# Performance work log

Measured on AMD Instinct MI355X. Metric: run time of the kernel, lower is better.

The kernel has to match this reference:

```python
import jax, jax.numpy as jnp
import numpy as np

TEMP = 0.02
KD_W = 1.0
VSD_W = 1.0
VLAD_W = 1.0
CON_W = 1.0
MSE_W = 1.0

B, SS, ST, DS, DT, V, NV, NT = 8, 96, 128, 1024, 2048, 32000, 32, 64


def hungarian(cost):
    # Shortest-augmenting-path assignment (e-maxx / Jonker-Volgenant style).
    # Square cost [n, n]; returns col_of_row so that row i matches column
    # col_of_row[i] with minimal total cost (same as scipy linear_sum_assignment).
    cost = np.asarray(cost, dtype=np.float64)
    n = cost.shape[0]
    INF = 1e18
    u = np.zeros(n + 1)
    v = np.zeros(n + 1)
    p = np.zeros(n + 1, dtype=np.int64)
    way = np.zeros(n + 1, dtype=np.int64)
    for i in range(1, n + 1):
        p[0] = i
        j0 = 0
        minv = np.full(n + 1, INF)
        used = np.zeros(n + 1, dtype=bool)
        while True:
            used[j0] = True
            i0 = p[j0]
            js = np.nonzero(~used)[0]
            js = js[js > 0]
            cur = cost[i0 - 1, js - 1] - u[i0] - v[js]
            upd = cur < minv[js]
            minv[js] = np.where(upd, cur, minv[js])
            way[js] = np.where(upd, j0, way[js])
            k = int(np.argmin(minv[js]))
            delta = minv[js][k]
            j1 = int(js[k])
            u[p[used]] += delta
            v[used] -= delta
            minv[~used] -= delta
            j0 = j1
            if p[j0] == 0:
                break
        while j0:
            j1 = int(way[j0])
            p[j0] = p[j1]
            j0 = j1
    col_of_row = np.zeros(n, dtype=np.int64)
    for j in range(1, n + 1):
        col_of_row[p[j] - 1] = j - 1
    return col_of_row


def _match(s_logits, t_logits):
    # Per-sample L1 (p=1 cdist) cost between teacher rows and student cols,
    # then Hungarian matching. Host-side loop is unavoidable (sequential
    # combinatorial algorithm), matching the original per-sample scipy loop.
    idx = []
    for b in range(s_logits.shape[0]):
        cost = np.abs(t_logits[b][:, None, :] - s_logits[b][None, :, :]).sum(-1)
        idx.append(hungarian(cost))
    return np.stack(idx)


def _cosine(a, b, eps=1e-8):
    # a: [B, M, D], b: [B, N, D] -> [B, M, N]; torch F.cosine_similarity semantics
    an = a / jnp.maximum(jnp.linalg.norm(a, axis=-1, keepdims=True), eps)
    bn = b / jnp.maximum(jnp.linalg.norm(b, axis=-1, keepdims=True), eps)
    return jnp.einsum('bmd,bnd->bmn', an, bn)


def setup_inputs() -> dict:
    key = jax.random.key(0)
    ks = jax.random.split(key, 12)
    f = jax.random.normal
    return {
        's_qry_reps': f(ks[0], (B, DS), jnp.float32),
        's_pos_reps': f(ks[1], (B, DS), jnp.float32),
        't_qry_reps': f(ks[2], (B, DT), jnp.float32),
        't_pos_reps': f(ks[3], (B, DT), jnp.float32),
        's_hidden_qry': f(ks[4], (B, SS, DS), jnp.float32),
        's_hidden_pos': f(ks[5], (B, SS, DS), jnp.float32),
        't_hidden_qry': f(ks[6], (B, ST, DT), jnp.float32),
        't_hidden_pos': f(ks[7], (B, ST, DT), jnp.float32),
        'W_s_lm': f(ks[8], (DS, V), jnp.float32) / np.float32(np.sqrt(DS)),
        'W_t_lm': f(ks[9], (DT, V), jnp.float32) / np.float32(np.sqrt(DT)),
        'W_proj': f(ks[10], (DT, DS), jnp.float32) / np.float32(np.sqrt(DT)),
        'b_proj': jnp.zeros((DS,), jnp.float32),
        'nv': NV,
        'nt': NT,
    }


def reference(s_qry_reps, s_pos_reps, t_qry_reps, t_pos_reps,
              s_hidden_qry, s_hidden_pos, t_hidden_qry, t_hidden_pos,
              W_s_lm, W_t_lm, W_proj, b_proj, nv, nt):
    Bn = s_qry_reps.shape[0]
    # 1) contrastive InfoNCE (world_size=1 -> gather is identity, target=arange)
    scores = (s_qry_reps @ s_pos_reps.T) / TEMP
    logp = jax.nn.log_softmax(scores, axis=-1)
    contrastive = -jnp.mean(jnp.diagonal(logp))
    # 2) MSE vs t2s-projected teacher reps
    mse = 0.5 * (jnp.mean((s_qry_reps - (t_qry_reps @ W_proj + b_proj)) ** 2)
                 + jnp.mean((s_pos_reps - (t_pos_reps @ W_proj + b_proj)) ** 2))
    # 3/4) VSD + VLAD over qry and pos sides stacked -> [2B, ...]
    s_hid = jnp.concatenate([s_hidden_qry, s_hidden_pos], axis=0)
    t_hid = jnp.concatenate([t_hidden_qry, t_hidden_pos], axis=0)
    St = t_hid.shape[1]
    sv = s_hid[:, :nv]                      # student vision tokens   [2B, Nv, DS]
    st = s_hid[:, nv:nv + nt]               # student text tokens     [2B, Nt, DS]
    tv = t_hid[:, St - nv - nt:St - nt]     # teacher vision tokens   [2B, Nv, DT]
    tt = t_hid[:, St - nt:]                 # teacher text tokens     [2B, Nt, DT]
    s_logits = jnp.einsum('bnd,dv->bnv', sv, W_s_lm)   # [2B, Nv, V]
    t_logits = jnp.einsum('bnd,dv->bnv', tv, W_t_lm)   # [2B, Nv, V]
    # Hungarian matching on detached logits (host side, like the original)
    idx = jnp.asarray(_match(np.asarray(s_logits), np.asarray(t_logits)))  # [2B, Nv]
    # VSD: MSE between matched student logits and teacher logits (t order = arange)
    s_logits_m = jnp.take_along_axis(s_logits, idx[:, :, None], axis=1)
    vsd = jnp.sum(jnp.mean((s_logits_m - t_logits) ** 2, axis=(1, 2)))
    # VLAD: smooth-L1 on vision->text cosine affinity maps
    sv_m = jnp.take_along_axis(sv, idx[:, :, None], axis=1)
    d = _cosine(sv_m, st) - _cosine(tv, tt)            # [2B, Nv, Nt]
    ad = jnp.abs(d)
    sl1 = jnp.where(ad < 1.0, 0.5 * d * d, ad - 0.5)
    vlad = jnp.sum(jnp.mean(sl1, axis=(1, 2)))
    distill = (VSD_W * vsd + VLAD_W * vlad) / Bn
    loss = CON_W * contrastive + MSE_W * mse + KD_W * distill
    return loss, contrastive, distill
```

## Files before the change

### kernel.cpp

```cpp
#include <hip/hip_runtime.h>
#include <math.h>

#define DS_ 1024
#define DT_ 2048
#define V_  32000
#define SS_ 96
#define ST_ 128


__device__ __forceinline__ float block_reduce_sum_256(float v) {
  __shared__ float tmp[4];
  #pragma unroll
  for (int off = 32; off; off >>= 1) v += __shfl_xor(v, off);
  const int wid = threadIdx.x >> 6;
  if ((threadIdx.x & 63) == 0) tmp[wid] = v;
  __syncthreads();
  if (threadIdx.x == 0) v = tmp[0] + tmp[1] + tmp[2] + tmp[3];
  return v;
}

__device__ __forceinline__ const float* s_base(int b, const float* s_hq, const float* s_hp) {
  return (b < 8) ? (s_hq + (size_t)b * SS_ * DS_) : (s_hp + (size_t)(b - 8) * SS_ * DS_);
}
__device__ __forceinline__ const float* t_base(int b, const float* t_hq, const float* t_hp) {
  return (b < 8) ? (t_hq + (size_t)b * ST_ * DT_) : (t_hp + (size_t)(b - 8) * ST_ * DT_);
}

__device__ __forceinline__ unsigned short f2bf(float x) {
  unsigned int u = __float_as_uint(x);
  u += 0x7fffu + ((u >> 16) & 1u);
  return (unsigned short)(u >> 16);
}
__device__ __forceinline__ float bf2f(unsigned short u) {
  return __uint_as_float(((unsigned int)u) << 16);
}

using bf16x8 = __attribute__((ext_vector_type(8))) short;
using f32x4  = __attribute__((ext_vector_type(4))) float;
using u16x4  = __attribute__((ext_vector_type(4))) unsigned short;

__device__ __forceinline__ void gll16(const void* g, void* l) {
  __builtin_amdgcn_global_load_lds((const __attribute__((address_space(1))) unsigned int*)g,
                                   (__attribute__((address_space(3))) unsigned int*)l, 16, 0, 0);
}

__device__ __forceinline__ unsigned int wave_umin_dpp(unsigned int r) {
  unsigned int t;
  t = (unsigned int)__builtin_amdgcn_update_dpp((int)r, (int)r, 0x111, 0xF, 0xF, false); r = r < t ? r : t;
  t = (unsigned int)__builtin_amdgcn_update_dpp((int)r, (int)r, 0x112, 0xF, 0xF, false); r = r < t ? r : t;
  t = (unsigned int)__builtin_amdgcn_update_dpp((int)r, (int)r, 0x114, 0xF, 0xF, false); r = r < t ? r : t;
  t = (unsigned int)__builtin_amdgcn_update_dpp((int)r, (int)r, 0x118, 0xF, 0xF, false); r = r < t ? r : t;
  t = (unsigned int)__builtin_amdgcn_update_dpp((int)r, (int)r, 0x142, 0xF, 0xF, false); r = r < t ? r : t;
  t = (unsigned int)__builtin_amdgcn_update_dpp((int)r, (int)r, 0x143, 0xF, 0xF, false); r = r < t ? r : t;
  return r;
}


__device__ __forceinline__ void scores_body(int blk, const float* __restrict__ sq,
                                            const float* __restrict__ sp,
                                            float* __restrict__ scores) {
  const int i = blk >> 3, j = blk & 7;
  float acc = 0.f;
  for (int k = threadIdx.x; k < DS_; k += 256)
    acc += sq[(size_t)i * DS_ + k] * sp[(size_t)j * DS_ + k];
  acc = block_reduce_sum_256(acc);
  if (threadIdx.x == 0) scores[i * 8 + j] = acc * 50.0f;
}

__device__ __forceinline__ void proj2_body(int kc, const float* __restrict__ t_qry,
                                           const float* __restrict__ t_pos,
                                           const float* __restrict__ Wp,
                                           float* __restrict__ proj,
                                           unsigned char* smem) {
  float (*tv)[64] = (float (*)[64])smem;
  const int tid = threadIdx.x;
  for (int s = tid; s < 16 * 64; s += 256) {
    const int zi = s >> 6, k = s & 63;
    const float* t = (zi >= 8) ? (t_pos + (size_t)(zi - 8) * DT_) : (t_qry + (size_t)zi * DT_);
    tv[zi][k] = t[kc * 64 + k];
  }
  __syncthreads();
  const int d4 = tid * 4;
  float4 acc[16];
  #pragma unroll
  for (int zi = 0; zi < 16; ++zi) acc[zi] = (float4){0.f, 0.f, 0.f, 0.f};
  for (int k = 0; k < 64; ++k) {
    const float4 w = *(const float4*)&Wp[(size_t)(kc * 64 + k) * DS_ + d4];
    #pragma unroll
    for (int zi = 0; zi < 16; ++zi) {
      const float t = tv[zi][k];
      acc[zi].x += t * w.x; acc[zi].y += t * w.y;
      acc[zi].z += t * w.z; acc[zi].w += t * w.w;
    }
  }
  #pragma unroll
  for (int zi = 0; zi < 16; ++zi) {
    float* p = proj + (size_t)zi * DS_ + d4;
    atomicAdd(&p[0], acc[zi].x); atomicAdd(&p[1], acc[zi].y);
    atomicAdd(&p[2], acc[zi].z); atomicAdd(&p[3], acc[zi].w);
  }
}

__device__ __forceinline__ void norms_body(int blk, const float* __restrict__ s_hq,
                                           const float* __restrict__ s_hp,
                                           const float* __restrict__ t_hq,
                                           const float* __restrict__ t_hp,
                                           float* __restrict__ invn) {
  const int b = blk / 192, t = blk % 192;
  const float* bs = s_base(b, s_hq, s_hp);
  const float* bt = t_base(b, t_hq, t_hp);
  const float* row;
  int K;
  float* out;
  if (t < 32)       { row = bs + (size_t)t * DS_;             K = DS_; out = invn + b * 32 + t; }
  else if (t < 96)  { row = bs + (size_t)t * DS_;             K = DS_; out = invn + 512 + b * 64 + (t - 32); }
  else if (t < 128) { row = bt + (size_t)(t - 96 + 32) * DT_;  K = DT_; out = invn + 1536 + b * 32 + (t - 96); }
  else              { row = bt + (size_t)(t - 128 + 64) * DT_; K = DT_; out = invn + 2048 + b * 64 + (t - 128); }
  float ss = 0.f;
  for (int k = threadIdx.x; k < K; k += 256) { const float x = row[k]; ss += x * x; }
  ss = block_reduce_sum_256(ss);
  if (threadIdx.x == 0) *out = 1.0f / fmaxf(sqrtf(ss), 1e-8f);
}

__device__ __forceinline__ void pack_as_body(int g, const float* __restrict__ s_hq,
                                             const float* __restrict__ s_hp,
                                             unsigned short* __restrict__ As) {
  const int b = g >> 5, i = g & 31;
  const float* src = s_base(b, s_hq, s_hp) + (size_t)i * DS_;
  const int k4 = threadIdx.x * 4;
  const float4 w = *(const float4*)&src[k4];
  u16x4 o; o[0] = f2bf(w.x); o[1] = f2bf(w.y); o[2] = f2bf(w.z); o[3] = f2bf(w.w);
  *(u16x4*)&As[(size_t)g * DS_ + k4] = o;
}

__device__ __forceinline__ void pack_at_body(int g, const float* __restrict__ t_hq,
                                             const float* __restrict__ t_hp,
                                             unsigned short* __restrict__ At) {
  const int b = g >> 5, i = g & 31;
  const float* src = t_base(b, t_hq, t_hp) + (size_t)(32 + i) * DT_;
  #pragma unroll
  for (int it = 0; it < 2; ++it) {
    const int k4 = (threadIdx.x + it * 256) * 4;
    const float4 w = *(const float4*)&src[k4];
    u16x4 o; o[0] = f2bf(w.x); o[1] = f2bf(w.y); o[2] = f2bf(w.z); o[3] = f2bf(w.w);
    *(u16x4*)&At[(size_t)g * DT_ + k4] = o;
  }
}

__device__ __forceinline__ void convw_body(int id, const float* __restrict__ W,
                                           unsigned short* __restrict__ Wbt,
                                           int K, unsigned char* smem) {
  float (*tile)[65] = (float (*)[65])smem;
  const int v0 = (id % 500) * 64, k0 = (id / 500) * 64;
  const int tid = threadIdx.x;
  #pragma unroll
  for (int it = 0; it < 4; ++it) {
    const int kr = (tid >> 4) + it * 16;
    const int v4 = (tid & 15) * 4;
    const float4 w = *(const float4*)&W[(size_t)(k0 + kr) * V_ + v0 + v4];
    tile[v4 + 0][kr] = w.x; tile[v4 + 1][kr] = w.y;
    tile[v4 + 2][kr] = w.z; tile[v4 + 3][kr] = w.w;
  }
  __syncthreads();
  #pragma unroll
  for (int it = 0; it < 2; ++it) {
    const int s = tid + it * 256;
    const int v = s >> 3, ch = s & 7;
    const float* src = &tile[v][ch * 8];
    unsigned int o[4];
    #pragma unroll
    for (int q = 0; q < 4; ++q)
      o[q] = (unsigned int)f2bf(src[2 * q]) | ((unsigned int)f2bf(src[2 * q + 1]) << 16);
    uint4 pk = {o[0], o[1], o[2], o[3]};
    *(uint4*)&Wbt[(size_t)(v0 + v) * K + k0 + ch * 8] = pk;
  }
}

__device__ __forceinline__ void dt_body(int id, const float* __restrict__ t_hq,
                                        const float* __restrict__ t_hp,
                                        float* __restrict__ dtd) {
  const int b = id >> 5, i = id & 31;
  const int wv = threadIdx.x >> 6, lane = threadIdx.x & 63;
  const float* bt = t_base(b, t_hq, t_hp);
  const float* a2p = bt + (size_t)(32 + i) * DT_;
  float a2[32];
  #pragma unroll
  for (int q = 0; q < 32; ++q) a2[q] = a2p[lane + 64 * q];
  for (int jj = 0; jj < 16; ++jj) {
    const int j = wv * 16 + jj;
    const float* b2 = bt + (size_t)(64 + j) * DT_;
    float dt = 0.f;
    #pragma unroll
    for (int q = 0; q < 32; ++q) dt += a2[q] * b2[lane + 64 * q];
    #pragma unroll
    for (int off = 32; off; off >>= 1) dt += __shfl_xor(dt, off);
    if (lane == 0) dtd[(b * 32 + i) * 64 + j] = dt;
  }
}

__device__ __forceinline__ void cs_body(int id, const float* __restrict__ s_hq,
                                        const float* __restrict__ s_hp,
                                        float* __restrict__ csd) {
  const int b = id >> 5, i = id & 31;
  const int wv = threadIdx.x >> 6, lane = threadIdx.x & 63;
  const float* bs = s_base(b, s_hq, s_hp);
  const float* a1p = bs + (size_t)i * DS_;
  float a1[16];
  #pragma unroll
  for (int q = 0; q < 16; ++q) a1[q] = a1p[lane + 64 * q];
  for (int jj = 0; jj < 16; ++jj) {
    const int j = wv * 16 + jj;
    const float* b1 = bs + (size_t)(32 + j) * DS_;
    float ds = 0.f;
    #pragma unroll
    for (int q = 0; q < 16; ++q) ds += a1[q] * b1[lane + 64 * q];
    #pragma unroll
    for (int off = 32; off; off >>= 1) ds += __shfl_xor(ds, off);
    if (lane == 0) csd[(b * 32 + i) * 64 + j] = ds;
  }
}

__device__ __forceinline__ void mse2_body(int blk, const float* __restrict__ s_qry,
                                          const float* __restrict__ s_pos,
                                          const float* __restrict__ proj,
                                          const float* __restrict__ bp,
                                          float* __restrict__ mse_acc) {
  const int z = blk >> 3, i = blk & 7;
  const float* s = (z ? s_pos : s_qry) + (size_t)i * DS_;
  const float* p = proj + ((size_t)z * 8 + i) * DS_;
  float ss = 0.f;
  for (int d = threadIdx.x; d < DS_; d += 256) {
    const float diff = s[d] - (p[d] + bp[d]);
    ss += diff * diff;
  }
  ss = block_reduce_sum_256(ss);
  if (threadIdx.x == 0) atomicAdd(mse_acc, ss);
}


template <int K>
__device__ __forceinline__ void gemm_body(int blk, int nwg,
                                          const unsigned short* __restrict__ A,
                                          const unsigned short* __restrict__ Wbt,
                                          unsigned short* __restrict__ Out,
                                          unsigned char* smem) {
  unsigned short* AldsB = (unsigned short*)smem;
  unsigned short* BldsB = (unsigned short*)(smem + 32768);
  const int q = nwg >> 3, r = nwg & 7;
  const int xcd = blk & 7, off = blk >> 3;
  const int sblk = (xcd < r ? xcd * (q + 1) : r * (q + 1) + (xcd - r) * q) + off;
  const int m0 = (sblk & 1) * 256;
  const int n0 = (sblk >> 1) * 128;
  const int tid = threadIdx.x;
  const int wv = tid >> 6, lane = tid & 63;
  const int lr = lane & 15, cc = lane >> 4;

  f32x4 acc[4][8];
  #pragma unroll
  for (int mf = 0; mf < 4; ++mf)
    #pragma unroll
    for (int nf = 0; nf < 8; ++nf) acc[mf][nf] = (f32x4){0.f, 0.f, 0.f, 0.f};

  constexpr int NT = K / 32;

  auto stage = [&](int kt, int buf) {
    #pragma unroll
    for (int it = 0; it < 4; ++it) {
      const int slot = it * 256 + tid;
      const int row = slot >> 2, cs = slot & 3;
      gll16(A + (size_t)(m0 + row) * K + kt * 32 + ((cs ^ ((row >> 1) & 3)) << 3),
            AldsB + (size_t)buf * 8192 + (size_t)(it * 256 + wv * 64) * 8);
    }
    #pragma unroll
    for (int it = 0; it < 2; ++it) {
      const int slot = it * 256 + tid;
      const int row = slot >> 2, cs = slot & 3;
      gll16(Wbt + (size_t)(n0 + row) * K + kt * 32 + ((cs ^ ((row >> 1) & 3)) << 3),
            BldsB + (size_t)buf * 4096 + (size_t)(it * 256 + wv * 64) * 8);
    }
  };

  stage(0, 0);
  if (NT > 1) stage(1, 1);
  for (int kt = 0; kt < NT; ++kt) {
    const int cur = kt & 1;
    if (kt >= 1 && kt + 1 < NT) stage(kt + 1, cur ^ 1);
    if (kt + 1 < NT) asm volatile("s_waitcnt vmcnt(6)" ::: "memory");
    else             asm volatile("s_waitcnt vmcnt(0)" ::: "memory");
    asm volatile("s_barrier" ::: "memory");
    bf16x8 af[4];
    #pragma unroll
    for (int mf = 0; mf < 4; ++mf) {
      const int row = wv * 64 + mf * 16 + lr;
      af[mf] = *(const bf16x8*)(AldsB + cur * 8192 + row * 32 + ((cc ^ ((row >> 1) & 3)) << 3));
    }
    __builtin_amdgcn_s_setprio(1);
    #pragma unroll
    for (int nf = 0; nf < 8; ++nf) {
      const int vr = nf * 16 + lr;
      const bf16x8 bfr = *(const bf16x8*)(BldsB + cur * 4096 + vr * 32 + ((cc ^ ((vr >> 1) & 3)) << 3));
      #pragma unroll
      for (int mf = 0; mf < 4; ++mf)
        acc[mf][nf] = __builtin_amdgcn_mfma_f32_16x16x32_bf16(af[mf], bfr, acc[mf][nf], 0, 0, 0);
    }
    __builtin_amdgcn_s_setprio(0);
    asm volatile("s_barrier" ::: "memory");
  }

  unsigned short* Olds = AldsB;
  #pragma unroll
  for (int h = 0; h < 2; ++h) {
    if (h) __syncthreads();
    #pragma unroll
    for (int mf = 0; mf < 4; ++mf)
      #pragma unroll
      for (int nf4 = 0; nf4 < 4; ++nf4) {
        const int nf = h * 4 + nf4;
        #pragma unroll
        for (int q2 = 0; q2 < 4; ++q2) {
          const int row = wv * 64 + mf * 16 + (lane >> 4) * 4 + q2;
          const int col = nf4 * 16 + lr;
          Olds[row * 64 + (col ^ (((row >> 2) & 3) << 4))] = f2bf(acc[mf][nf][q2]);
        }
      }
    __syncthreads();
    #pragma unroll
    for (int it = 0; it < 4; ++it) {
      const int slot = it * 256 + tid;
      const int row = slot >> 3, c2 = slot & 7;
      const uint4 pk = *(const uint4*)&Olds[row * 64 + ((c2 ^ (((row >> 2) & 3) << 1)) << 3)];
      *(uint4*)&Out[(size_t)(m0 + row) * V_ + n0 + h * 64 + c2 * 8] = pk;
    }
  }
}


__global__ __launch_bounds__(256) void fused_pre_kernel(const float* __restrict__ s_qry,
                                                        const float* __restrict__ s_pos,
                                                        const float* __restrict__ t_qry,
                                                        const float* __restrict__ t_pos,
                                                        const float* __restrict__ s_hq,
                                                        const float* __restrict__ s_hp,
                                                        const float* __restrict__ t_hq,
                                                        const float* __restrict__ t_hp,
                                                        const float* __restrict__ Ws,
                                                        const float* __restrict__ Wp,
                                                        float* __restrict__ scores,
                                                        float* __restrict__ proj,
                                                        float* __restrict__ invn,
                                                        unsigned short* __restrict__ As,
                                                        unsigned short* __restrict__ At,
                                                        unsigned short* __restrict__ Wsb,
                                                        float* __restrict__ csd,
                                                        float* __restrict__ dtd) {
  __shared__ __align__(16) unsigned char smem[16640];
  const int blk = blockIdx.x;
  if (blk < 64)            scores_body(blk, s_qry, s_pos, scores);
  else if (blk < 96)       proj2_body(blk - 64, t_qry, t_pos, Wp, proj, smem);
  else if (blk < 3168)     norms_body(blk - 96, s_hq, s_hp, t_hq, t_hp, invn);
  else if (blk < 3680)     pack_as_body(blk - 3168, s_hq, s_hp, As);
  else if (blk < 4192)     pack_at_body(blk - 3680, t_hq, t_hp, At);
  else if (blk < 12192)    convw_body(blk - 4192, Ws, Wsb, DS_, smem);
  else if (blk < 12704)    cs_body(blk - 12192, s_hq, s_hp, csd);
  else                     dt_body(blk - 12704, t_hq, t_hp, dtd);
}

__global__ __launch_bounds__(256) void fused_mid_kernel(const unsigned short* __restrict__ As,
                                                        const unsigned short* __restrict__ Wsb,
                                                        unsigned short* __restrict__ Sg,
                                                        const float* __restrict__ Wt,
                                                        unsigned short* __restrict__ Wtb,
                                                        const float* __restrict__ s_qry,
                                                        const float* __restrict__ s_pos,
                                                        const float* __restrict__ proj,
                                                        const float* __restrict__ bp,
                                                        float* __restrict__ mse_acc) {
  __shared__ __align__(16) unsigned char smem[49152];
  const int blk = blockIdx.x;
  if (blk < 500)            gemm_body<DS_>(blk, 500, As, Wsb, Sg, smem);
  else if (blk < 16500)     convw_body(blk - 500, Wt, Wtb, DT_, smem);
  else                      mse2_body(blk - 16500, s_qry, s_pos, proj, bp, mse_acc);
}

__global__ __launch_bounds__(256) void gemm_tn_kernel_t(const unsigned short* __restrict__ A,
                                                        const unsigned short* __restrict__ Wbt,
                                                        unsigned short* __restrict__ Out) {
  __shared__ __align__(16) unsigned char smem[49152];
  gemm_body<DT_>(blockIdx.x, (int)gridDim.x, A, Wbt, Out, smem);
}


#define CPV 500
#define CPP 508

__global__ __launch_bounds__(256) void cost_pairs_kernel(const unsigned short* __restrict__ Sg,
                                                         const unsigned short* __restrict__ Tg,
                                                         float* __restrict__ cost1,
                                                         float* __restrict__ cost2) {
  __shared__ __align__(16) unsigned short Sl[32 * CPP];
  __shared__ __align__(16) unsigned short Tl[32 * CPP];
  const int b = blockIdx.x >> 6, sl = blockIdx.x & 63;
  const int v0 = sl * CPV;
  const int tid = threadIdx.x;

  for (int s = tid; s < 32 * 125; s += 256) {
    const int r = s / 125, c = s % 125;
    *(u16x4*)&Sl[r * CPP + c * 4] = *(const u16x4*)&Sg[(size_t)(b * 32 + r) * V_ + v0 + c * 4];
    *(u16x4*)&Tl[r * CPP + c * 4] = *(const u16x4*)&Tg[(size_t)(b * 32 + r) * V_ + v0 + c * 4];
  }
  __syncthreads();

  const int i = tid >> 3, j4 = (tid & 7) * 4;
  float a1[4] = {0.f, 0.f, 0.f, 0.f}, a2[4] = {0.f, 0.f, 0.f, 0.f};
  for (int v = 0; v < CPV; v += 4) {
    const u16x4 t4 = *(const u16x4*)&Tl[i * CPP + v];
    float tf[4];
    #pragma unroll
    for (int q = 0; q < 4; ++q) tf[q] = bf2f(t4[q]);
    #pragma unroll
    for (int jj = 0; jj < 4; ++jj) {
      const u16x4 s4 = *(const u16x4*)&Sl[(j4 + jj) * CPP + v];
      #pragma unroll
      for (int q = 0; q < 4; ++q) {
        const float d = tf[q] - bf2f(s4[q]);
        a1[jj] += fabsf(d);
        a2[jj] += d * d;
      }
    }
  }
  #pragma unroll
  for (int jj = 0; jj < 4; ++jj) {
    atomicAdd(&cost1[(size_t)b * 1024 + i * 32 + j4 + jj], a1[jj]);
    atomicAdd(&cost2[(size_t)b * 1024 + i * 32 + j4 + jj], a2[jj]);
  }
}


__global__ __launch_bounds__(64) void hungarian_kernel(const float* __restrict__ cost1,
                                                       const float* __restrict__ cost2,
                                                       int* __restrict__ idx,
                                                       float* __restrict__ vsd_acc) {
  const int b = blockIdx.x;
  const int lane = threadIdx.x;
  const float INF = __int_as_float(0x7f800000);
  __shared__ float C[32 * 33];
  __shared__ float u_lds[33];

  for (int s = lane; s < 1024; s += 64) {
    const int r = s >> 5, c = s & 31;
    C[r * 33 + c] = cost1[(size_t)b * 1024 + s];
  }
  if (lane == 0) u_lds[0] = 0.f;
  __syncthreads();

  const bool isj = (lane >= 1 && lane <= 32);
  const int cix = isj ? (lane - 1) : 0;

  if (lane < 32) {
    float m = C[lane * 33];
    for (int j = 1; j < 32; ++j) m = fminf(m, C[lane * 33 + j]);
    u_lds[lane + 1] = m;
  }
  __syncthreads();

  float v = 0.f;
  if (isj) {
    float m = INF;
    for (int i = 0; i < 32; ++i) m = fminf(m, C[i * 33 + cix] - u_lds[i + 1]);
    v = m;
  }

  int p = 0;
  unsigned int assigned = 0;
  for (int i = 1; i <= 32; ++i) {
    const float ui = u_lds[i];
    const bool zero = isj && (p == 0) && ((C[(i - 1) * 33 + cix] - ui) == v);
    const unsigned long long tie = __ballot(zero);
    if (tie) {
      const int j1 = __ffsll(tie) - 1;
      if (lane == j1) p = i;
      assigned |= (1u << (i - 1));
    }
  }

  for (int i = 1; i <= 32; ++i) {
    if (assigned & (1u << (i - 1))) continue;
    if (lane == 0) p = i;
    float minv = INF;
    int way = 0;
    int used = 0;
    int j0 = 0;
    float ui0 = u_lds[i];
    float crow = C[(i - 1) * 33 + cix];
    while (true) {
      if (lane == j0) used = 1;
      float val = INF;
      if (isj && !used) {
        const float cur = crow - ui0 - v;
        if (cur < minv) { minv = cur; way = j0; }
        val = minv;
      }
      const unsigned int rb = wave_umin_dpp(__float_as_uint(val));
      const unsigned int minb = (unsigned int)__builtin_amdgcn_readlane((int)rb, 63);
      const float delta = __uint_as_float(minb);
      const unsigned long long tie = __ballot(__float_as_uint(val) == minb);
      const int j1 = __ffsll(tie) - 1;
      const int i0n = __builtin_amdgcn_readlane(p, j1);
      const float ui0n = u_lds[i0n];
      const int nri = (i0n >= 1 ? i0n : 1) - 1;
      const float cnext = C[nri * 33 + cix];
      if (used) {
        u_lds[p] += delta;
        v -= delta;
      } else {
        minv -= delta;
      }
      j0 = j1;
      if (i0n == 0) break;
      ui0 = ui0n;
      crow = cnext;
    }
    while (j0) {
      const int j1 = __builtin_amdgcn_readlane(way, j0);
      const int pv = __builtin_amdgcn_readlane(p, j1);
      if (lane == j0) p = pv;
      j0 = j1;
    }
  }
  float term = 0.f;
  if (isj) {
    idx[b * 32 + (p - 1)] = lane - 1;
    term = cost2[(size_t)b * 1024 + (p - 1) * 32 + (lane - 1)];
  }
  #pragma unroll
  for (int off = 32; off; off >>= 1) term += __shfl_xor(term, off);
  if (lane == 0) atomicAdd(vsd_acc, term);
}


__global__ __launch_bounds__(256) void vlad_gather_kernel(const int* __restrict__ idx,
                                                          const float* __restrict__ invn,
                                                          const float* __restrict__ csd,
                                                          const float* __restrict__ dtd,
                                                          float* __restrict__ vlad_acc) {
  const int b = blockIdx.x;
  float local = 0.f;
  #pragma unroll
  for (int w = 0; w < 8; ++w) {
    const int cell = threadIdx.x * 8 + w;
    const int i = cell >> 6, j = cell & 63;
    const int is = idx[b * 32 + i];
    const float cs = csd[(b * 32 + is) * 64 + j] * invn[b * 32 + is] * invn[512 + b * 64 + j];
    const float ct = dtd[(b * 32 + i) * 64 + j] * invn[1536 + b * 32 + i] * invn[2048 + b * 64 + j];
    const float d = cs - ct;
    const float ad = fabsf(d);
    local += (ad < 1.f) ? 0.5f * d * d : ad - 0.5f;
  }
  local = block_reduce_sum_256(local);
  if (threadIdx.x == 0) atomicAdd(vlad_acc, local);
}


__global__ __launch_bounds__(64) void final_kernel(const float* __restrict__ scores,
                                                   const float* __restrict__ accs,
                                                   float* __restrict__ out) {
  const int lane = threadIdx.x;
  float ci = 0.f;
  if (lane < 8) {
    float m = -1e30f;
    for (int j = 0; j < 8; ++j) m = fmaxf(m, scores[lane * 8 + j]);
    float sum = 0.f;
    for (int j = 0; j < 8; ++j) sum += expf(scores[lane * 8 + j] - m);
    const float lse = m + logf(sum);
    ci = scores[lane * 8 + lane] - lse;
  }
  #pragma unroll
  for (int off = 32; off; off >>= 1) ci += __shfl_xor(ci, off);
  if (lane == 0) {
    const float contrastive = -ci / 8.0f;
    const float mse = accs[0] / 16384.0f;
    const float vsd = accs[1] / 1024000.0f;
    const float vlad = accs[2] / 2048.0f;
    const float distill = (vsd + vlad) / 8.0f;
    out[0] = contrastive + mse + distill;
    out[1] = contrastive;
    out[2] = distill;
  }
}


extern "C" void kernel_launch(void* const* d_in, const int* in_sizes, int n_in,
                              void* d_out, int out_size, void* d_ws, size_t ws_size,
                              hipStream_t stream) {
  const float* s_qry = (const float*)d_in[0];
  const float* s_pos = (const float*)d_in[1];
  const float* t_qry = (const float*)d_in[2];
  const float* t_pos = (const float*)d_in[3];
  const float* s_hq  = (const float*)d_in[4];
  const float* s_hp  = (const float*)d_in[5];
  const float* t_hq  = (const float*)d_in[6];
  const float* t_hp  = (const float*)d_in[7];
  const float* Ws    = (const float*)d_in[8];
  const float* Wt    = (const float*)d_in[9];
  const float* Wp    = (const float*)d_in[10];
  const float* bp    = (const float*)d_in[11];

  float* ws     = (float*)d_ws;
  float* scores = ws;
  float* cost1  = ws + 64;
  float* cost2  = ws + 16448;
  float* invn   = ws + 32832;
  float* accs   = ws + 35904;
  float* proj   = ws + 35908;
  int*   idx    = (int*)(ws + 52292);
  float* csd    = ws + 52804;
  float* dtd    = ws + 85572;
  const size_t small_bytes = (size_t)52804 * 4;

  const size_t As_off = 524288;
  const size_t At_off = As_off + (size_t)512 * DS_ * 2;
  const size_t Ws_off = At_off + (size_t)512 * DT_ * 2;
  const size_t Wt_off = Ws_off + (size_t)V_ * DS_ * 2;
  const size_t Sg_off = Wt_off + (size_t)V_ * DT_ * 2;
  const size_t Tg_off = Sg_off + (size_t)512 * V_ * 2;
  const size_t req2   = Tg_off + (size_t)512 * V_ * 2;

  hipMemsetAsync(d_ws, 0, small_bytes, stream);

  if (ws_size >= req2) {
    unsigned short* As  = (unsigned short*)((char*)d_ws + As_off);
    unsigned short* At  = (unsigned short*)((char*)d_ws + At_off);
    unsigned short* Wsb = (unsigned short*)((char*)d_ws + Ws_off);
    unsigned short* Wtb = (unsigned short*)((char*)d_ws + Wt_off);
    unsigned short* Sg  = (unsigned short*)((char*)d_ws + Sg_off);
    unsigned short* Tg  = (unsigned short*)((char*)d_ws + Tg_off);

    fused_pre_kernel<<<13216, 256, 0, stream>>>(s_qry, s_pos, t_qry, t_pos,
                                                s_hq, s_hp, t_hq, t_hp,
                                                Ws, Wp, scores, proj, invn,
                                                As, At, Wsb, csd, dtd);

    fused_mid_kernel<<<16516, 256, 0, stream>>>(As, Wsb, Sg, Wt, Wtb,
                                                s_qry, s_pos, proj, bp, accs + 0);

    gemm_tn_kernel_t<<<(V_ / 128) * 2, 256, 0, stream>>>(At, Wtb, Tg);
    cost_pairs_kernel<<<16 * 64, 256, 0, stream>>>(Sg, Tg, cost1, cost2);

    hungarian_kernel<<<16, 64, 0, stream>>>(cost1, cost2, idx, accs + 1);
    vlad_gather_kernel<<<16, 256, 0, stream>>>(idx, invn, csd, dtd, accs + 2);
    final_kernel<<<1, 64, 0, stream>>>(scores, accs, (float*)d_out);
  }
}
```

Before: 429.1 us.

## Regroup kernels into two dependency levels and fuse Hungarian with VLAD gather

Moves both weight bf16 conversions (Wt and Ws) into the first fused kernel, so the second fused kernel can run the student and teacher logit GEMMs together with the MSE blocks. This removes one launch and the serialization between the student GEMM and the teacher GEMM. It also folds the VLAD gather into the Hungarian kernel, keeping the matching indices in LDS instead of a global buffer, which drops another launch. In exchange the first kernel becomes much larger, and the 500-block teacher GEMM now waits for all conversion work to finish.

Measured after the change: 432.9 us, median of 2. Within noise of the previous version (+0.9%).

```diff
diff --git a/kernel.cpp b/kernel.cpp
--- a/kernel.cpp
+++ b/kernel.cpp
@@ -335,58 +335,55 @@
 }
 
 
-__global__ __launch_bounds__(256) void fused_pre_kernel(const float* __restrict__ s_qry,
-                                                        const float* __restrict__ s_pos,
-                                                        const float* __restrict__ t_qry,
-                                                        const float* __restrict__ t_pos,
-                                                        const float* __restrict__ s_hq,
-                                                        const float* __restrict__ s_hp,
-                                                        const float* __restrict__ t_hq,
-                                                        const float* __restrict__ t_hp,
-                                                        const float* __restrict__ Ws,
-                                                        const float* __restrict__ Wp,
-                                                        float* __restrict__ scores,
-                                                        float* __restrict__ proj,
-                                                        float* __restrict__ invn,
-                                                        unsigned short* __restrict__ As,
-                                                        unsigned short* __restrict__ At,
-                                                        unsigned short* __restrict__ Wsb,
-                                                        float* __restrict__ csd,
-                                                        float* __restrict__ dtd) {
+__global__ __launch_bounds__(256) void fused_l0_kernel(const float* __restrict__ s_qry,
+                                                       const float* __restrict__ s_pos,
+                                                       const float* __restrict__ t_qry,
+                                                       const float* __restrict__ t_pos,
+                                                       const float* __restrict__ s_hq,
+                                                       const float* __restrict__ s_hp,
+                                                       const float* __restrict__ t_hq,
+                                                       const float* __restrict__ t_hp,
+                                                       const float* __restrict__ Ws,
+                                                       const float* __restrict__ Wt,
+                                                       const float* __restrict__ Wp,
+                                                       float* __restrict__ scores,
+                                                       float* __restrict__ proj,
+                                                       float* __restrict__ invn,
+                                                       unsigned short* __restrict__ As,
+                                                       unsigned short* __restrict__ At,
+                                                       unsigned short* __restrict__ Wsb,
+                                                       unsigned short* __restrict__ Wtb,
+                                                       float* __restrict__ csd,
+                                                       float* __restrict__ dtd) {
   __shared__ __align__(16) unsigned char smem[16640];
   const int blk = blockIdx.x;
-  if (blk < 64)            scores_body(blk, s_qry, s_pos, scores);
-  else if (blk < 96)       proj2_body(blk - 64, t_qry, t_pos, Wp, proj, smem);
-  else if (blk < 3168)     norms_body(blk - 96, s_hq, s_hp, t_hq, t_hp, invn);
-  else if (blk < 3680)     pack_as_body(blk - 3168, s_hq, s_hp, As);
-  else if (blk < 4192)     pack_at_body(blk - 3680, t_hq, t_hp, At);
-  else if (blk < 12192)    convw_body(blk - 4192, Ws, Wsb, DS_, smem);
-  else if (blk < 12704)    cs_body(blk - 12192, s_hq, s_hp, csd);
-  else                     dt_body(blk - 12704, t_hq, t_hp, dtd);
-}
-
-__global__ __launch_bounds__(256) void fused_mid_kernel(const unsigned short* __restrict__ As,
-                                                        const unsigned short* __restrict__ Wsb,
-                                                        unsigned short* __restrict__ Sg,
-                                                        const float* __restrict__ Wt,
-                                                        unsigned short* __restrict__ Wtb,
-                                                        const float* __restrict__ s_qry,
-                                                        const float* __restrict__ s_pos,
-                                                        const float* __restrict__ proj,
-                                                        const float* __restrict__ bp,
-                                                        float* __restrict__ mse_acc) {
+  if (blk < 16000)         convw_body(blk, Wt, Wtb, DT_, smem);
+  else if (blk < 24000)    convw_body(blk - 16000, Ws, Wsb, DS_, smem);
+  else if (blk < 24064)    scores_body(blk - 24000, s_qry, s_pos, scores);
+  else if (blk < 24096)    proj2_body(blk - 24064, t_qry, t_pos, Wp, proj, smem);
+  else if (blk < 27168)    norms_body(blk - 24096, s_hq, s_hp, t_hq, t_hp, invn);
+  else if (blk < 27680)    pack_as_body(blk - 27168, s_hq, s_hp, As);
+  else if (blk < 28192)    pack_at_body(blk - 27680, t_hq, t_hp, At);
+  else if (blk < 28704)    cs_body(blk - 28192, s_hq, s_hp, csd);
+  else                     dt_body(blk - 28704, t_hq, t_hp, dtd);
+}
+
+__global__ __launch_bounds__(256) void fused_l1_kernel(const unsigned short* __restrict__ As,
+                                                       const unsigned short* __restrict__ Wsb,
+                                                       unsigned short* __restrict__ Sg,
+                                                       const unsigned short* __restrict__ At,
+                                                       const unsigned short* __restrict__ Wtb,
+                                                       unsigned short* __restrict__ Tg,
+                                                       const float* __restrict__ s_qry,
+                                                       const float* __restrict__ s_pos,
+                                                       const float* __restrict__ proj,
+                                                       const float* __restrict__ bp,
+                                                       float* __restrict__ mse_acc) {
   __shared__ __align__(16) unsigned char smem[49152];
   const int blk = blockIdx.x;
-  if (blk < 500)            gemm_body<DS_>(blk, 500, As, Wsb, Sg, smem);
-  else if (blk < 16500)     convw_body(blk - 500, Wt, Wtb, DT_, smem);
-  else                      mse2_body(blk - 16500, s_qry, s_pos, proj, bp, mse_acc);
-}
-
-__global__ __launch_bounds__(256) void gemm_tn_kernel_t(const unsigned short* __restrict__ A,
-                                                        const unsigned short* __restrict__ Wbt,
-                                                        unsigned short* __restrict__ Out) {
-  __shared__ __align__(16) unsigned char smem[49152];
-  gemm_body<DT_>(blockIdx.x, (int)gridDim.x, A, Wbt, Out, smem);
+  if (blk < 500)            gemm_body<DT_>(blk, 500, At, Wtb, Tg, smem);
+  else if (blk < 1000)      gemm_body<DS_>(blk - 500, 500, As, Wsb, Sg, smem);
+  else                      mse2_body(blk - 1000, s_qry, s_pos, proj, bp, mse_acc);
 }
 
 
@@ -436,120 +433,119 @@
 }
 
 
-__global__ __launch_bounds__(64) void hungarian_kernel(const float* __restrict__ cost1,
-                                                       const float* __restrict__ cost2,
-                                                       int* __restrict__ idx,
-                                                       float* __restrict__ vsd_acc) {
+__global__ __launch_bounds__(256) void hung_vlad_kernel(const float* __restrict__ cost1,
+                                                        const float* __restrict__ cost2,
+                                                        const float* __restrict__ invn,
+                                                        const float* __restrict__ csd,
+                                                        const float* __restrict__ dtd,
+                                                        float* __restrict__ vsd_acc,
+                                                        float* __restrict__ vlad_acc) {
   const int b = blockIdx.x;
-  const int lane = threadIdx.x;
+  const int tid = threadIdx.x;
   const float INF = __int_as_float(0x7f800000);
   __shared__ float C[32 * 33];
   __shared__ float u_lds[33];
-
-  for (int s = lane; s < 1024; s += 64) {
+  __shared__ int idx_lds[32];
+
+  for (int s = tid; s < 1024; s += 256) {
     const int r = s >> 5, c = s & 31;
     C[r * 33 + c] = cost1[(size_t)b * 1024 + s];
   }
-  if (lane == 0) u_lds[0] = 0.f;
+  if (tid == 0) u_lds[0] = 0.f;
   __syncthreads();
-
-  const bool isj = (lane >= 1 && lane <= 32);
-  const int cix = isj ? (lane - 1) : 0;
-
-  if (lane < 32) {
-    float m = C[lane * 33];
-    for (int j = 1; j < 32; ++j) m = fminf(m, C[lane * 33 + j]);
-    u_lds[lane + 1] = m;
+  if (tid < 32) {
+    float m = C[tid * 33];
+    for (int j = 1; j < 32; ++j) m = fminf(m, C[tid * 33 + j]);
+    u_lds[tid + 1] = m;
   }
   __syncthreads();
 
-  float v = 0.f;
-  if (isj) {
-    float m = INF;
-    for (int i = 0; i < 32; ++i) m = fminf(m, C[i * 33 + cix] - u_lds[i + 1]);
-    v = m;
-  }
-
-  int p = 0;
-  unsigned int assigned = 0;
-  for (int i = 1; i <= 32; ++i) {
-    const float ui = u_lds[i];
-    const bool zero = isj && (p == 0) && ((C[(i - 1) * 33 + cix] - ui) == v);
-    const unsigned long long tie = __ballot(zero);
-    if (tie) {
-      const int j1 = __ffsll(tie) - 1;
-      if (lane == j1) p = i;
-      assigned |= (1u << (i - 1));
-    }
-  }
-
-  for (int i = 1; i <= 32; ++i) {
-    if (assigned & (1u << (i - 1))) continue;
-    if (lane == 0) p = i;
-    float minv = INF;
-    int way = 0;
-    int used = 0;
-    int j0 = 0;
-    float ui0 = u_lds[i];
-    float crow = C[(i - 1) * 33 + cix];
-    while (true) {
-      if (lane == j0) used = 1;
-      float val = INF;
-      if (isj && !used) {
-        const float cur = crow - ui0 - v;
-        if (cur < minv) { minv = cur; way = j0; }
-        val = minv;
+  if (tid < 64) {
+    const int lane = tid;
+    const bool isj = (lane >= 1 && lane <= 32);
+    const int cix = isj ? (lane - 1) : 0;
+
+    float v = 0.f;
+    if (isj) {
+      float m = INF;
+      for (int i = 0; i < 32; ++i) m = fminf(m, C[i * 33 + cix] - u_lds[i + 1]);
+      v = m;
+    }
+
+    int p = 0;
+    unsigned int assigned = 0;
+    for (int i = 1; i <= 32; ++i) {
+      const float ui = u_lds[i];
+      const bool zero = isj && (p == 0) && ((C[(i - 1) * 33 + cix] - ui) == v);
+      const unsigned long long tie = __ballot(zero);
+      if (tie) {
+        const int j1 = __ffsll(tie) - 1;
+        if (lane == j1) p = i;
+        assigned |= (1u << (i - 1));
       }
-      const unsigned int rb = wave_umin_dpp(__float_as_uint(val));
-      const unsigned int minb = (unsigned int)__builtin_amdgcn_readlane((int)rb, 63);
-      const float delta = __uint_as_float(minb);
-      const unsigned long long tie = __ballot(__float_as_uint(val) == minb);
-      const int j1 = __ffsll(tie) - 1;
-      const int i0n = __builtin_amdgcn_readlane(p, j1);
-      const float ui0n = u_lds[i0n];
-      const int nri = (i0n >= 1 ? i0n : 1) - 1;
-      const float cnext = C[nri * 33 + cix];
-      if (used) {
-        u_lds[p] += delta;
-        v -= delta;
-      } else {
-        minv -= delta;
+    }
+
+    for (int i = 1; i <= 32; ++i) {
+      if (assigned & (1u << (i - 1))) continue;
+      if (lane == 0) p = i;
+      float minv = INF;
+      int way = 0;
+      int used = 0;
+      int j0 = 0;
+      float ui0 = u_lds[i];
+      float crow = C[(i - 1) * 33 + cix];
+      while (true) {
+        if (lane == j0) used = 1;
+        float val = INF;
+        if (isj && !used) {
+          const float cur = crow - ui0 - v;
+          if (cur < minv) { minv = cur; way = j0; }
+          val = minv;
+        }
+        const unsigned int rb = wave_umin_dpp(__float_as_uint(val));
+        const unsigned int minb = (unsigned int)__builtin_amdgcn_readlane((int)rb, 63);
+        const float delta = __uint_as_float(minb);
+        const unsigned long long tie = __ballot(__float_as_uint(val) == minb);
+        const int j1 = __ffsll(tie) - 1;
+        const int i0n = __builtin_amdgcn_readlane(p, j1);
+        const float ui0n = u_lds[i0n];
+        const int nri = (i0n >= 1 ? i0n : 1) - 1;
+        const float cnext = C[nri * 33 + cix];
+        if (used) {
+          u_lds[p] += delta;
+          v -= delta;
+        } else {
+          minv -= delta;
+        }
+        j0 = j1;
+        if (i0n == 0) break;
+        ui0 = ui0n;
+        crow = cnext;
       }
-      j0 = j1;
-      if (i0n == 0) break;
-      ui0 = ui0n;
-      crow = cnext;
-    }
-    while (j0) {
-      const int j1 = __builtin_amdgcn_readlane(way, j0);
-      const int pv = __builtin_amdgcn_readlane(p, j1);
-      if (lane == j0) p = pv;
-      j0 = j1;
-    }
-  }
-  float term = 0.f;
-  if (isj) {
-    idx[b * 32 + (p - 1)] = lane - 1;
-    term = cost2[(size_t)b * 1024 + (p - 1) * 32 + (lane - 1)];
-  }
-  #pragma unroll
-  for (int off = 32; off; off >>= 1) term += __shfl_xor(term, off);
-  if (lane == 0) atomicAdd(vsd_acc, term);
-}
-
-
-__global__ __launch_bounds__(256) void vlad_gather_kernel(const int* __restrict__ idx,
-                                                          const float* __restrict__ invn,
-                                                          const float* __restrict__ csd,
-                                                          const float* __restrict__ dtd,
-                                                          float* __restrict__ vlad_acc) {
-  const int b = blockIdx.x;
+      while (j0) {
+        const int j1 = __builtin_amdgcn_readlane(way, j0);
+        const int pv = __builtin_amdgcn_readlane(p, j1);
+        if (lane == j0) p = pv;
+        j0 = j1;
+      }
+    }
+    float term = 0.f;
+    if (isj) {
+      idx_lds[p - 1] = lane - 1;
+      term = cost2[(size_t)b * 1024 + (p - 1) * 32 + (lane - 1)];
+    }
+    #pragma unroll
+    for (int off = 32; off; off >>= 1) term += __shfl_xor(term, off);
+    if (lane == 0) atomicAdd(vsd_acc, term);
+  }
+  __syncthreads();
+
   float local = 0.f;
   #pragma unroll
   for (int w = 0; w < 8; ++w) {
-    const int cell = threadIdx.x * 8 + w;
+    const int cell = tid * 8 + w;
     const int i = cell >> 6, j = cell & 63;
-    const int is = idx[b * 32 + i];
+    const int is = idx_lds[i];
     const float cs = csd[(b * 32 + is) * 64 + j] * invn[b * 32 + is] * invn[512 + b * 64 + j];
     const float ct = dtd[(b * 32 + i) * 64 + j] * invn[1536 + b * 32 + i] * invn[2048 + b * 64 + j];
     const float d = cs - ct;
@@ -557,7 +553,7 @@
     local += (ad < 1.f) ? 0.5f * d * d : ad - 0.5f;
   }
   local = block_reduce_sum_256(local);
-  if (threadIdx.x == 0) atomicAdd(vlad_acc, local);
+  if (tid == 0) atomicAdd(vlad_acc, local);
 }
 
 
@@ -612,10 +608,9 @@
   float* invn   = ws + 32832;
   float* accs   = ws + 35904;
   float* proj   = ws + 35908;
-  int*   idx    = (int*)(ws + 52292);
-  float* csd    = ws + 52804;
-  float* dtd    = ws + 85572;
-  const size_t small_bytes = (size_t)52804 * 4;
+  float* csd    = ws + 52292;
+  float* dtd    = ws + 85060;
+  const size_t small_bytes = (size_t)52292 * 4;
 
   const size_t As_off = 524288;
   const size_t At_off = As_off + (size_t)512 * DS_ * 2;
@@ -635,19 +630,18 @@
     unsigned short* Sg  = (unsigned short*)((char*)d_ws + Sg_off);
     unsigned short* Tg  = (unsigned short*)((char*)d_ws + Tg_off);
 
-    fused_pre_kernel<<<13216, 256, 0, stream>>>(s_qry, s_pos, t_qry, t_pos,
-                                                s_hq, s_hp, t_hq, t_hp,
-                                                Ws, Wp, scores, proj, invn,
-                                                As, At, Wsb, csd, dtd);
-
-    fused_mid_kernel<<<16516, 256, 0, stream>>>(As, Wsb, Sg, Wt, Wtb,
-                                                s_qry, s_pos, proj, bp, accs + 0);
-
-    gemm_tn_kernel_t<<<(V_ / 128) * 2, 256, 0, stream>>>(At, Wtb, Tg);
+    fused_l0_kernel<<<29216, 256, 0, stream>>>(s_qry, s_pos, t_qry, t_pos,
+                                               s_hq, s_hp, t_hq, t_hp,
+                                               Ws, Wt, Wp, scores, proj, invn,
+                                               As, At, Wsb, Wtb, csd, dtd);
+
+    fused_l1_kernel<<<1016, 256, 0, stream>>>(As, Wsb, Sg, At, Wtb, Tg,
+                                              s_qry, s_pos, proj, bp, accs + 0);
+
     cost_pairs_kernel<<<16 * 64, 256, 0, stream>>>(Sg, Tg, cost1, cost2);
 
-    hungarian_kernel<<<16, 64, 0, stream>>>(cost1, cost2, idx, accs + 1);
-    vlad_gather_kernel<<<16, 256, 0, stream>>>(idx, invn, csd, dtd, accs + 2);
+    hung_vlad_kernel<<<16, 256, 0, stream>>>(cost1, cost2, invn, csd, dtd,
+                                             accs + 1, accs + 2);
     final_kernel<<<1, 64, 0, stream>>>(scores, accs, (float*)d_out);
   }
 }
```
